# Kernel tuning notes

Hardware: AMD Instinct MI355X
Metric: run time of the kernel (lower is better)

## Reference

```python
import jax, jax.numpy as jnp
import numpy as np

BS, NS, NCP, NH, C, HID, R = 8, 2048, 8, 8, 128, 128, 128


def rotation_6d_to_matrix(d6):
    a1, a2 = d6[..., :3], d6[..., 3:]
    b1 = a1 / jnp.linalg.norm(a1, axis=-1, keepdims=True)
    b2 = a2 - jnp.sum(b1 * a2, axis=-1, keepdims=True) * b1
    b2 = b2 / jnp.linalg.norm(b2, axis=-1, keepdims=True)
    b3 = jnp.cross(b1, b2)
    return jnp.stack([b1, b2, b3], axis=-2)  # (..., 3, 3), rows b1,b2,b3


def _sample_plane(plane, uv):
    # plane: (B,C,R,R); uv: (B,N,2) in [0,1]; uv[...,0]->width, uv[...,1]->height
    Rr = plane.shape[-1]
    x = jnp.clip(uv[..., 0], 0.0, 1.0) * (Rr - 1)
    y = jnp.clip(uv[..., 1], 0.0, 1.0) * (Rr - 1)
    x0 = jnp.floor(x); y0 = jnp.floor(y)
    wx = x - x0; wy = y - y0
    x0i = x0.astype(jnp.int32); y0i = y0.astype(jnp.int32)
    x1i = jnp.minimum(x0i + 1, Rr - 1); y1i = jnp.minimum(y0i + 1, Rr - 1)
    gb = jax.vmap(lambda p, yi, xi: p[:, yi, xi])  # per-batch gather -> (C,N)
    f00 = gb(plane, y0i, x0i); f01 = gb(plane, y0i, x1i)
    f10 = gb(plane, y1i, x0i); f11 = gb(plane, y1i, x1i)
    wx = wx[:, None, :]; wy = wy[:, None, :]
    f = f00 * (1 - wx) * (1 - wy) + f01 * wx * (1 - wy) + f10 * (1 - wx) * wy + f11 * wx * wy
    return jnp.transpose(f, (0, 2, 1))  # (B,N,C)


def triplane_sample(p, pxz, pxy, pyz):
    # p: (B,N,3) in [0,1]^3; sum of bilinear samples from the three planes
    return (_sample_plane(pxz, p[..., jnp.array([0, 2])])
            + _sample_plane(pxy, p[..., jnp.array([0, 1])])
            + _sample_plane(pyz, p[..., jnp.array([1, 2])]))


def setup_inputs() -> dict:
    key = jax.random.key(0)
    ks = jax.random.split(key, 10)
    s = 1.0 / np.sqrt(C)
    return {
        "query_pos": jax.random.uniform(ks[0], (BS, NS, 9), dtype=jnp.float32),
        "plane_xz": jax.random.normal(ks[1], (BS, C, R, R), dtype=jnp.float32),
        "plane_xy": jax.random.normal(ks[2], (BS, C, R, R), dtype=jnp.float32),
        "plane_yz": jax.random.normal(ks[3], (BS, C, R, R), dtype=jnp.float32),
        "control_points": jax.random.normal(ks[4], (NCP, 3), dtype=jnp.float32) * 0.05,
        "W_v": jax.random.normal(ks[5], (C, HID), dtype=jnp.float32) * s,
        "b_v": jnp.zeros((HID,), jnp.float32),
        "W_w": jax.random.normal(ks[6], (C, NCP * NH), dtype=jnp.float32) * s,
        "b_w": jnp.zeros((NCP * NH,), jnp.float32),
        "W_o": jax.random.normal(ks[7], (HID, C), dtype=jnp.float32) * s,
        "b_o": jnp.zeros((C,), jnp.float32),
    }


def reference(query_pos, plane_xz, plane_xy, plane_yz, control_points,
              W_v, b_v, W_w, b_w, W_o, b_o):
    bs, ns, _ = query_pos.shape
    q_ori = query_pos[..., 3:]
    q_pos = query_pos[..., :3]
    feature = triplane_sample(q_pos, plane_xz, plane_xy, plane_yz)  # (bs,ns,C)
    rot = rotation_6d_to_matrix(q_ori)  # (bs,ns,3,3)
    # rotate control points: einsum('bnpd,bngd->bngp') with cp broadcast over (bs,ns)
    cp = jnp.einsum('bnpd,gd->bngp', rot, control_points)  # (bs,ns,ncp,3)
    anchor = q_pos[:, :, None, :] + cp  # (bs,ns,ncp,3)
    sf = triplane_sample(anchor.reshape(bs, ns * NCP, 3), plane_xz, plane_xy, plane_yz)
    sf = sf.reshape(bs * ns, NCP, C)  # head dim in torch code is a pure repeat
    feat = feature.reshape(bs * ns, C)
    w = (feat @ W_w + b_w).reshape(bs * ns, NCP, NH)  # (B,ncp,heads)
    vbase = sf @ W_v + b_v  # (B,ncp,hid); identical across repeated head dim
    # torch: (v * weights).sum((1,2)) with v_t[b,i,j,k]=vbase[b,j,k], w[b,i,j]
    out = jnp.einsum('bjk,bij->bk', vbase, w)  # (B,hid)
    out = out @ W_o + b_o
    out = out + feat
    return out.reshape(bs, ns, -1)
```

## Files before the change

### kernel.cpp

```cpp
#include <hip/hip_runtime.h>
#include <hip/hip_fp16.h>
#include <math.h>

constexpr int BS  = 8;
constexpr int NS  = 2048;
constexpr int NCP = 8;
constexpr int NH  = 8;
constexpr int C   = 128;
constexpr int HID = 128;
constexpr int RR  = 128;

constexpr int QPB = 8;
constexpr int VEC = 4;

constexpr int NPOS = RR * RR;
constexpr size_t PLE = (size_t)BS * NPOS * C;

constexpr int TPOS   = 64;
constexpr int NBLK_T = 3 * BS * (NPOS / TPOS);

__host__ __device__ __forceinline__ int ch_of_slot(int s) {
    return (s >> 3) + ((s & 7) << 4);
}
__host__ __device__ __forceinline__ int slot_of_ch(int c) {
    return ((c & 15) << 3) | (c >> 4);
}

typedef __attribute__((address_space(3))) float lds_f;
typedef const __attribute__((address_space(1))) float glb_f;

struct F4 { float x, y, z, w; };
__device__ __forceinline__ F4 f4add(F4 a, F4 b) {
    return F4{a.x + b.x, a.y + b.y, a.z + b.z, a.w + b.w};
}
__device__ __forceinline__ F4 f4fma(F4 acc, float s, F4 v) {
    return F4{fmaf(s, v.x, acc.x), fmaf(s, v.y, acc.y),
              fmaf(s, v.z, acc.z), fmaf(s, v.w, acc.w)};
}
__device__ __forceinline__ F4 cvt4(int2 r) {
    __half2 h0 = *reinterpret_cast<__half2*>(&r.x);
    __half2 h1 = *reinterpret_cast<__half2*>(&r.y);
    float2 f0 = __half22float2(h0);
    float2 f1 = __half22float2(h1);
    return F4{f0.x, f0.y, f1.x, f1.y};
}

__global__ __launch_bounds__(256) void trans_prep_k(
    const float* __restrict__ pxz, const float* __restrict__ pxy,
    const float* __restrict__ pyz, __half* __restrict__ dst,
    const float* __restrict__ Wv, const float* __restrict__ bv,
    const float* __restrict__ Ww, const float* __restrict__ bw,
    const float* __restrict__ Wo,
    float* __restrict__ Wf, float* __restrict__ bf,
    float* __restrict__ Ww2, float* __restrict__ bw2)
{
    const int bid = blockIdx.x;
    const int t   = threadIdx.x;

    if (bid >= NBLK_T) {
        const int k = bid - NBLK_T;
        const int c = t;
        if (c >= 128) return;
        if (k < 128) {
            const int kk = ch_of_slot(k);
            float acc = 0.f;
            #pragma unroll 8
            for (int j = 0; j < 128; ++j) acc += Wv[kk * 128 + j] * Wo[j * 128 + c];
            Wf[k * 128 + c] = acc;
        } else if (k == 128) {
            float acc = 0.f;
            #pragma unroll 8
            for (int j = 0; j < 128; ++j) acc += bv[j] * Wo[j * 128 + c];
            bf[c] = acc;
        } else {
            const int cc = ch_of_slot(c);
            float s[NH];
            #pragma unroll
            for (int h = 0; h < NH; ++h) s[h] = 0.f;
            #pragma unroll
            for (int i = 0; i < NCP; ++i)
                #pragma unroll
                for (int h = 0; h < NH; ++h) s[h] += Ww[cc * (NCP * NH) + i * NH + h];
            #pragma unroll
            for (int h = 0; h < NH; ++h) Ww2[c * NH + h] = s[h];
            if (c < NH) {
                float tt = 0.f;
                #pragma unroll
                for (int i = 0; i < NCP; ++i) tt += bw[i * NH + c];
                bw2[c] = tt;
            }
        }
        return;
    }

    const int b    = bid & 7;
    const int idx  = bid >> 3;
    const int pl   = idx >> 8;
    const int tile = idx & 255;
    const int n0   = tile * TPOS;

    const float* src = (pl == 0 ? pxz : (pl == 1 ? pxy : pyz))
                       + (size_t)b * C * NPOS;
    __half* d = dst + (size_t)(pl * BS + b) * ((size_t)NPOS * C);

    __shared__ float lds[C * TPOS];

    const int wave = t >> 6;
    const int lane = t & 63;
    const int cw   = lane >> 4;
    const int blk  = lane & 15;

    #pragma unroll
    for (int j = 0; j < 8; ++j) {
        const int c0 = wave * 32 + j * 4;
        const int c  = c0 + cw;
        const int sb = blk ^ (c & 15);
        glb_f* gp = (glb_f*)(src + (size_t)c * NPOS + n0 + sb * 4);
        lds_f* lp = (lds_f*)(&lds[c0 * TPOS]);
        __builtin_amdgcn_global_load_lds(gp, lp, 16, 0, 0);
    }
    __syncthreads();

    #pragma unroll
    for (int i = 0; i < 4; ++i) {
        const int li = i * 256 + t;
        const int n  = li >> 4;
        const int g  = li & 15;
        const int ro = (((n >> 2) ^ g) << 2) + (n & 3);
        unsigned u[4];
        #pragma unroll
        for (int jj = 0; jj < 4; ++jj) {
            const float vA = lds[(g + 32 * jj) * TPOS + ro];
            const float vB = lds[(g + 32 * jj + 16) * TPOS + ro];
            __half2 h = __floats2half2_rn(vA, vB);
            u[jj] = *reinterpret_cast<unsigned*>(&h);
        }
        *reinterpret_cast<uint4*>(d + (size_t)(n0 + n) * C + g * 8) =
            make_uint4(u[0], u[1], u[2], u[3]);
    }
}

__device__ __forceinline__ F4 samp(const __half* __restrict__ base, float u, float v)
{
    float x = fminf(fmaxf(u, 0.f), 1.f) * (float)(RR - 1);
    float y = fminf(fmaxf(v, 0.f), 1.f) * (float)(RR - 1);
    float x0f = floorf(x), y0f = floorf(y);
    float wx = x - x0f, wy = y - y0f;
    int x0 = (int)x0f, y0 = (int)y0f;
    int x1 = min(x0 + 1, RR - 1), y1 = min(y0 + 1, RR - 1);
    int r0 = y0 << 14, r1 = y1 << 14, cc0 = x0 << 7, cc1 = x1 << 7;
    int2 a00 = *reinterpret_cast<const int2*>(base + r0 + cc0);
    int2 a01 = *reinterpret_cast<const int2*>(base + r0 + cc1);
    int2 a10 = *reinterpret_cast<const int2*>(base + r1 + cc0);
    int2 a11 = *reinterpret_cast<const int2*>(base + r1 + cc1);
    float w00 = (1.f - wx) * (1.f - wy), w01 = wx * (1.f - wy);
    float w10 = (1.f - wx) * wy,         w11 = wx * wy;
    F4 f00 = cvt4(a00), f01 = cvt4(a01), f10 = cvt4(a10), f11 = cvt4(a11);
    F4 r;
    r.x = f00.x * w00 + f01.x * w01 + f10.x * w10 + f11.x * w11;
    r.y = f00.y * w00 + f01.y * w01 + f10.y * w10 + f11.y * w11;
    r.z = f00.z * w00 + f01.z * w01 + f10.z * w10 + f11.z * w11;
    r.w = f00.w * w00 + f01.w * w01 + f10.w * w10 + f11.w * w11;
    return r;
}

__global__ __launch_bounds__(256) void attn_k(
    const float* __restrict__ qpos,
    const __half* __restrict__ planes,
    const float* __restrict__ cpts,
    const float* __restrict__ Ww2, const float* __restrict__ bw2,
    const float* __restrict__ Wf,  const float* __restrict__ bf,
    const float* __restrict__ bo,
    float* __restrict__ out)
{
    const int nb   = gridDim.x;
    const int cpx  = nb >> 3;
    const int sbid = (blockIdx.x & 7) * cpx + (blockIdx.x >> 3);

    const int tid  = threadIdx.x;
    const int ql   = tid >> 5;
    const int lane = tid & 31;
    const int c4   = lane * VEC;
    const int q    = sbid * QPB + ql;
    const int b    = q >> 11;

    const float* qp = qpos + (size_t)q * 9;
    const float px = qp[0], py = qp[1], pz = qp[2];
    const float a1x = qp[3], a1y = qp[4], a1z = qp[5];
    const float a2x = qp[6], a2y = qp[7], a2z = qp[8];

    float inv = 1.f / sqrtf(a1x * a1x + a1y * a1y + a1z * a1z);
    float b1x = a1x * inv, b1y = a1y * inv, b1z = a1z * inv;
    float dd  = b1x * a2x + b1y * a2y + b1z * a2z;
    float b2x = a2x - dd * b1x, b2y = a2y - dd * b1y, b2z = a2z - dd * b1z;
    inv = 1.f / sqrtf(b2x * b2x + b2y * b2y + b2z * b2z);
    b2x *= inv; b2y *= inv; b2z *= inv;
    float b3x = b1y * b2z - b1z * b2y;
    float b3y = b1z * b2x - b1x * b2z;
    float b3z = b1x * b2y - b1y * b2x;

    const __half* Pxz = planes + (size_t)b * ((size_t)NPOS * C) + c4;
    const __half* Pxy = Pxz + PLE;
    const __half* Pyz = Pxy + PLE;

    F4 feat = f4add(f4add(samp(Pxz, px, pz), samp(Pxy, px, py)), samp(Pyz, py, pz));

    float p[NH];
    #pragma unroll
    for (int h = 0; h < NH; ++h) p[h] = 0.f;
    {
        const float* wr = Ww2 + c4 * NH;
        const float fv[VEC] = {feat.x, feat.y, feat.z, feat.w};
        #pragma unroll
        for (int i = 0; i < VEC; ++i)
            #pragma unroll
            for (int h = 0; h < NH; ++h) p[h] += fv[i] * wr[i * NH + h];
    }
    #pragma unroll
    for (int off = 16; off >= 1; off >>= 1)
        #pragma unroll
        for (int h = 0; h < NH; ++h) p[h] += __shfl_xor(p[h], off);

    float ws[NH], Ssum = 0.f;
    #pragma unroll
    for (int h = 0; h < NH; ++h) { ws[h] = p[h] + bw2[h]; Ssum += ws[h]; }

    F4 comb = {0.f, 0.f, 0.f, 0.f};
    #pragma unroll 2
    for (int g = 0; g < NCP; ++g) {
        float cx = cpts[g * 3 + 0], cy = cpts[g * 3 + 1], cz = cpts[g * 3 + 2];
        float ax = px + b1x * cx + b1y * cy + b1z * cz;
        float ay = py + b2x * cx + b2y * cy + b2z * cz;
        float az = pz + b3x * cx + b3y * cy + b3z * cz;
        F4 s = f4add(f4add(samp(Pxz, ax, az), samp(Pxy, ax, ay)), samp(Pyz, ay, az));
        comb = f4fma(comb, ws[g], s);
    }

    __shared__ float sComb[QPB][C];
    __shared__ float sFeat[QPB][C];
    __shared__ float sSum[QPB];
    *reinterpret_cast<float4*>(&sComb[ql][c4]) = make_float4(comb.x, comb.y, comb.z, comb.w);
    *reinterpret_cast<float4*>(&sFeat[ql][c4]) = make_float4(feat.x, feat.y, feat.z, feat.w);
    if (lane == 0) sSum[ql] = Ssum;
    __syncthreads();

    const int c  = tid & 127;
    const int sl = slot_of_ch(c);
    const int q0 = (tid >> 7) * 4;
    float acc[4];
    const float bfc = bf[c], boc = bo[c];
    #pragma unroll
    for (int j = 0; j < 4; ++j)
        acc[j] = sSum[q0 + j] * bfc + boc + sFeat[q0 + j][sl];
    #pragma unroll 4
    for (int k = 0; k < C; ++k) {
        float wf = Wf[k * C + c];
        #pragma unroll
        for (int j = 0; j < 4; ++j) acc[j] += sComb[q0 + j][k] * wf;
    }
    #pragma unroll
    for (int j = 0; j < 4; ++j)
        out[(size_t)(sbid * QPB + q0 + j) * C + c] = acc[j];
}

extern "C" void kernel_launch(void* const* d_in, const int* in_sizes, int n_in,
                              void* d_out, int out_size, void* d_ws, size_t ws_size,
                              hipStream_t stream)
{
    const float* qpos = (const float*)d_in[0];
    const float* pxz  = (const float*)d_in[1];
    const float* pxy  = (const float*)d_in[2];
    const float* pyz  = (const float*)d_in[3];
    const float* cpts = (const float*)d_in[4];
    const float* Wv   = (const float*)d_in[5];
    const float* bv   = (const float*)d_in[6];
    const float* Ww   = (const float*)d_in[7];
    const float* bw   = (const float*)d_in[8];
    const float* Wo   = (const float*)d_in[9];
    const float* bo   = (const float*)d_in[10];
    float* out = (float*)d_out;

    __half* plh = (__half*)d_ws;
    float*  wsf = (float*)((char*)d_ws + 3 * PLE * sizeof(__half));
    float* Wf  = wsf;
    float* bf  = Wf + C * HID;
    float* Ww2 = bf + C;
    float* bw2 = Ww2 + C * NH;

    hipLaunchKernelGGL(trans_prep_k, dim3(NBLK_T + 130), dim3(256), 0, stream,
                       pxz, pxy, pyz, plh, Wv, bv, Ww, bw, Wo, Wf, bf, Ww2, bw2);

    hipLaunchKernelGGL(attn_k, dim3(BS * NS / QPB), dim3(256), 0, stream,
                       qpos, plh, cpts, Ww2, bw2, Wf, bf, bo, out);
}
```

Before: 120.2 us.

## Retile plane transpose into 64-channel by 512-position blocks with new channel permutation

The fp32-to-fp16 plane transpose kernel now processes tiles of 64 channels by 512 positions instead of 128 channels by 64 positions, giving fewer, larger blocks with longer contiguous global reads per channel. The channel-slot permutation is changed to match, so each store writes 8-byte chunks into half of a position's channel vector. LDS use grows to 128 KB per block, which limits occupancy, and the output stores are narrower than the previous 16-byte writes.

```diff
diff --git a/kernel.cpp b/kernel.cpp
--- a/kernel.cpp
+++ b/kernel.cpp
@@ -16,14 +16,15 @@
 constexpr int NPOS = RR * RR;
 constexpr size_t PLE = (size_t)BS * NPOS * C;
 
-constexpr int TPOS   = 64;
-constexpr int NBLK_T = 3 * BS * (NPOS / TPOS);
-
+constexpr int CHB    = 64;
+constexpr int PB     = 512;
+constexpr int NBLK_T = 3 * BS * (C / CHB) * (NPOS / PB);
+
+__host__ __device__ __forceinline__ int slot_of_ch(int c) {
+    return (c & 64) | ((c & 15) << 2) | ((c >> 4) & 3);
+}
 __host__ __device__ __forceinline__ int ch_of_slot(int s) {
-    return (s >> 3) + ((s & 7) << 4);
-}
-__host__ __device__ __forceinline__ int slot_of_ch(int c) {
-    return ((c & 15) << 3) | (c >> 4);
+    return (s & 64) | ((s & 3) << 4) | ((s >> 2) & 15);
 }
 
 typedef __attribute__((address_space(3))) float lds_f;
@@ -54,6 +55,8 @@
     float* __restrict__ Wf, float* __restrict__ bf,
     float* __restrict__ Ww2, float* __restrict__ bw2)
 {
+    __shared__ float lds[CHB * PB];
+
     const int bid = blockIdx.x;
     const int t   = threadIdx.x;
 
@@ -93,50 +96,50 @@
         return;
     }
 
-    const int b    = bid & 7;
-    const int idx  = bid >> 3;
-    const int pl   = idx >> 8;
-    const int tile = idx & 255;
-    const int n0   = tile * TPOS;
+    const int b   = bid & 7;
+    const int idx = bid >> 3;
+    const int pl  = idx >> 6;
+    const int r   = idx & 63;
+    const int cg  = r & 1;
+    const int pg  = r >> 1;
+    const int c0  = cg * CHB;
+    const int n0  = pg * PB;
 
     const float* src = (pl == 0 ? pxz : (pl == 1 ? pxy : pyz))
-                       + (size_t)b * C * NPOS;
+                       + (size_t)b * C * NPOS + (size_t)c0 * NPOS;
     __half* d = dst + (size_t)(pl * BS + b) * ((size_t)NPOS * C);
-
-    __shared__ float lds[C * TPOS];
 
     const int wave = t >> 6;
     const int lane = t & 63;
-    const int cw   = lane >> 4;
-    const int blk  = lane & 15;
-
-    #pragma unroll
-    for (int j = 0; j < 8; ++j) {
-        const int c0 = wave * 32 + j * 4;
-        const int c  = c0 + cw;
-        const int sb = blk ^ (c & 15);
-        glb_f* gp = (glb_f*)(src + (size_t)c * NPOS + n0 + sb * 4);
-        lds_f* lp = (lds_f*)(&lds[c0 * TPOS]);
+
+    #pragma unroll
+    for (int k = 0; k < 32; ++k) {
+        const int cl   = wave * 16 + (k >> 1);
+        const int half = k & 1;
+        const int s    = cl & 15;
+        glb_f* gp = (glb_f*)(src + (size_t)cl * NPOS + n0
+                             + (((half << 6) + (lane ^ s)) << 2));
+        lds_f* lp = (lds_f*)(&lds[cl * PB + half * 256]);
         __builtin_amdgcn_global_load_lds(gp, lp, 16, 0, 0);
     }
     __syncthreads();
 
     #pragma unroll
-    for (int i = 0; i < 4; ++i) {
-        const int li = i * 256 + t;
+    for (int it = 0; it < 32; ++it) {
+        const int li = it * 256 + t;
         const int n  = li >> 4;
         const int g  = li & 15;
-        const int ro = (((n >> 2) ^ g) << 2) + (n & 3);
-        unsigned u[4];
-        #pragma unroll
-        for (int jj = 0; jj < 4; ++jj) {
-            const float vA = lds[(g + 32 * jj) * TPOS + ro];
-            const float vB = lds[(g + 32 * jj + 16) * TPOS + ro];
-            __half2 h = __floats2half2_rn(vA, vB);
-            u[jj] = *reinterpret_cast<unsigned*>(&h);
-        }
-        *reinterpret_cast<uint4*>(d + (size_t)(n0 + n) * C + g * 8) =
-            make_uint4(u[0], u[1], u[2], u[3]);
+        const int bp = (((n >> 2) ^ g) << 2) + (n & 3);
+        float f[4];
+        #pragma unroll
+        for (int j = 0; j < 4; ++j)
+            f[j] = lds[(g + 16 * j) * PB + bp];
+        __half2 h01 = __floats2half2_rn(f[0], f[1]);
+        __half2 h23 = __floats2half2_rn(f[2], f[3]);
+        uint2 v;
+        v.x = *reinterpret_cast<unsigned*>(&h01);
+        v.y = *reinterpret_cast<unsigned*>(&h23);
+        *reinterpret_cast<uint2*>(d + (size_t)(n0 + n) * C + c0 + g * 4) = v;
     }
 }
 
```

Measured after the change: 126.5 us. 5.2% more time.
